# Kernel optimization log

Measured on AMD Instinct MI355X. Metric: run time of the kernel, lower is better.

Reference implementation:

```python
import jax, jax.numpy as jnp
import numpy as np

B, N, H = 8192, 8, 1024  # batch, DOF, hidden width; state dim = 2*N


def setup_inputs() -> dict:
    key = jax.random.key(0)
    ks = jax.random.split(key, 4)
    s1 = 1.0 / np.sqrt(2 * N)
    s2 = 1.0 / np.sqrt(H)
    return {
        "x": jax.random.normal(ks[0], (B, 2 * N), dtype=jnp.float32),
        "W1": jax.random.normal(ks[1], (2 * N, H), dtype=jnp.float32) * s1,
        "b1": jnp.zeros((H,), dtype=jnp.float32),
        "W2": jax.random.normal(ks[2], (H, H), dtype=jnp.float32) * s2,
        "b2": jnp.zeros((H,), dtype=jnp.float32),
        "W3": jax.random.normal(ks[3], (H, 1), dtype=jnp.float32) * s2,
        "b3": jnp.zeros((1,), dtype=jnp.float32),
    }


def reference(x, W1, b1, W2, b2, W3, b3):
    def lagrangian(q, qd):
        z = jnp.concatenate([q, qd])           # (2N,)
        h = jax.nn.softplus(z @ W1 + b1)
        h = jax.nn.softplus(h @ W2 + b2)
        return (h @ W3 + b3).sum()             # scalar L(q, qd)

    dL_dq_fn = jax.grad(lagrangian, argnums=0)
    dL_dqd_fn = jax.grad(lagrangian, argnums=1)
    # forward-over-reverse Hessian blocks (cheap: only N tangents)
    H_qdqd_fn = jax.jacfwd(dL_dqd_fn, argnums=1)   # d2L/dqd dqd, (N,N)
    H_qddq_fn = jax.jacfwd(dL_dqd_fn, argnums=0)   # d2L/dqd dq,  (N,N)

    def step(xi):
        q, qd = xi[:N], xi[N:]
        dL_dq = dL_dq_fn(q, qd)                      # (N,)
        M = H_qdqd_fn(q, qd)                         # mass-matrix block
        C = H_qddq_fn(q, qd)
        qdd = jnp.linalg.inv(M) @ (dL_dq - C @ qd)   # (N,)
        return jnp.concatenate([qd, qdd])            # (2N,)

    return jax.vmap(step)(x)
```

## Files before the change

### kernel.cpp

```cpp
#include <hip/hip_runtime.h>
#include <math.h>

#define B_ 8192
#define H_ 1024
#define LDP0 136
#define LDT 148

#define A_SEC 145
#define B2_SEC 257
#define A_GRN (12*A_SEC)
#define B2_GRN (12*B2_SEC)
#define AB2_SH ((A_GRN + B2_GRN)*8)

typedef short bfrag __attribute__((ext_vector_type(8)));
typedef float f4v  __attribute__((ext_vector_type(4)));

union U8 { unsigned short u[8]; uint4 v; };

__device__ __forceinline__ float sigf(float x){ return 1.0f/(1.0f+__expf(-x)); }

__device__ __forceinline__ unsigned int pkhi(unsigned int u1, unsigned int u0){
  return __builtin_amdgcn_perm(u1, u0, 0x07060302u);
}

__device__ __forceinline__ void gload_lds16(const void* g, void* l){
  __builtin_amdgcn_global_load_lds(
      (const __attribute__((address_space(1))) void*)g,
      (__attribute__((address_space(3))) void*)l, 16, 0, 0);
}

__global__ void k1_s1(const float* __restrict__ x, const float* __restrict__ W1,
                      const float* __restrict__ b1, float* __restrict__ s1o){
  __shared__ float xs[16];
  int b = blockIdx.x, t = threadIdx.x;
  if(t < 16) xs[t] = x[b*16 + t];
  __syncthreads();
  for(int h = t; h < H_; h += 256){
    float acc = b1[h];
    #pragma unroll
    for(int j=0;j<16;j++) acc = __fmaf_rn(xs[j], W1[j*H_ + h], acc);
    s1o[(size_t)b*H_ + h] = sigf(acc);
  }
}

__global__ __launch_bounds__(256,3) void k2_s2(const float* __restrict__ s1,
                      const float* __restrict__ W2, const float* __restrict__ b2,
                      float* __restrict__ s2o){
  __shared__ __align__(16) float As[32*LDP0];
  __shared__ __align__(16) float Bs[32*LDP0];
  int t = threadIdx.x, tx = t & 15, ty = t >> 4;
  int m0 = blockIdx.x * 128, n0 = blockIdx.y * 128;
  int jj = t & 31, rb4 = (t >> 5) * 4;
  float acc[8][8];
  #pragma unroll
  for(int i=0;i<8;i++){
    #pragma unroll
    for(int k=0;k<8;k++) acc[i][k]=0.f; }

  for(int jt=0; jt<32; jt++){
    int j0 = jt*32;
    __syncthreads();
    #pragma unroll
    for(int g=0; g<4; g++){
      #pragma unroll
      for(int i=0;i<4;i++){
        int r = rb4 + i + 32*g;
        As[jj*LDP0 + r] = -__logf(1.0f - s1[(size_t)(m0+r)*H_ + j0 + jj]);
      }
    }
    { int jB = t >> 3, kb = (t & 7) * 16;
      const float* src = &W2[(size_t)(j0 + jB)*H_ + n0 + kb];
      #pragma unroll
      for(int c=0;c<4;c++) *(float4*)&Bs[jB*LDP0 + kb + 4*c] = *(const float4*)(src + 4*c);
    }
    __syncthreads();
    #pragma unroll 8
    for(int j=0;j<32;j++){
      float4 a0 = *(const float4*)&As[j*LDP0 + 8*ty];
      float4 a1f= *(const float4*)&As[j*LDP0 + 8*ty+4];
      float4 b0 = *(const float4*)&Bs[j*LDP0 + 4*tx];
      float4 b1f= *(const float4*)&Bs[j*LDP0 + 64 + 4*tx];
      float aa[8] = {a0.x,a0.y,a0.z,a0.w,a1f.x,a1f.y,a1f.z,a1f.w};
      float bb[8] = {b0.x,b0.y,b0.z,b0.w,b1f.x,b1f.y,b1f.z,b1f.w};
      #pragma unroll
      for(int i=0;i<8;i++){
        #pragma unroll
        for(int k=0;k<8;k++) acc[i][k] = __fmaf_rn(aa[i], bb[k], acc[i][k]); }
    }
  }
  float4 bb0 = *(const float4*)&b2[n0 + 4*tx];
  float4 bb1 = *(const float4*)&b2[n0 + 64 + 4*tx];
  #pragma unroll
  for(int i=0;i<8;i++){
    size_t r = (size_t)(m0 + 8*ty + i)*H_;
    float4 o0 = make_float4(sigf(acc[i][0]+bb0.x), sigf(acc[i][1]+bb0.y),
                            sigf(acc[i][2]+bb0.z), sigf(acc[i][3]+bb0.w));
    float4 o1 = make_float4(sigf(acc[i][4]+bb1.x), sigf(acc[i][5]+bb1.y),
                            sigf(acc[i][6]+bb1.z), sigf(acc[i][7]+bb1.w));
    *(float4*)&s2o[r + n0 + 4*tx] = o0;
    *(float4*)&s2o[r + n0 + 64 + 4*tx] = o1;
  }
}

__global__ __launch_bounds__(256,3) void k3_u(const float* __restrict__ s2,
                      const float* __restrict__ W2, const float* __restrict__ W3,
                      float* __restrict__ u){
  __shared__ __align__(16) float As[32*LDP0];
  __shared__ __align__(16) float Bs[32*LDP0];
  int t = threadIdx.x, tx = t & 15, ty = t >> 4;
  int m0 = blockIdx.x * 128, n0 = blockIdx.y * 128;
  int jj = t & 31, rb4 = (t >> 5) * 4;
  float acc[8][8];
  #pragma unroll
  for(int i=0;i<8;i++){
    #pragma unroll
    for(int k=0;k<8;k++) acc[i][k]=0.f; }

  for(int kt=0; kt<32; kt++){
    int k0 = kt*32;
    __syncthreads();
    float w3v = W3[k0 + jj];
    #pragma unroll
    for(int g=0; g<4; g++){
      #pragma unroll
      for(int i=0;i<4;i++){
        int r = rb4 + i + 32*g;
        As[jj*LDP0 + r] = w3v * s2[(size_t)(m0+r)*H_ + k0 + jj];
      }
    }
    { int jcol = t >> 1, kb = (t & 1) * 16;
      const float* src = &W2[(size_t)(n0 + jcol)*H_ + k0 + kb];
      #pragma unroll
      for(int c=0;c<16;c++) Bs[(kb+c)*LDP0 + jcol] = src[c];
    }
    __syncthreads();
    #pragma unroll 8
    for(int j=0;j<32;j++){
      float4 a0 = *(const float4*)&As[j*LDP0 + 8*ty];
      float4 a1f= *(const float4*)&As[j*LDP0 + 8*ty+4];
      float4 b0 = *(const float4*)&Bs[j*LDP0 + 4*tx];
      float4 b1f= *(const float4*)&Bs[j*LDP0 + 64 + 4*tx];
      float aa[8] = {a0.x,a0.y,a0.z,a0.w,a1f.x,a1f.y,a1f.z,a1f.w};
      float bb[8] = {b0.x,b0.y,b0.z,b0.w,b1f.x,b1f.y,b1f.z,b1f.w};
      #pragma unroll
      for(int i=0;i<8;i++){
        #pragma unroll
        for(int k=0;k<8;k++) acc[i][k] = __fmaf_rn(aa[i], bb[k], acc[i][k]); }
    }
  }
  #pragma unroll
  for(int i=0;i<8;i++){
    size_t r = (size_t)(m0 + 8*ty + i)*H_;
    *(float4*)&u[r + n0 + 4*tx]      = make_float4(acc[i][0],acc[i][1],acc[i][2],acc[i][3]);
    *(float4*)&u[r + n0 + 64 + 4*tx] = make_float4(acc[i][4],acc[i][5],acc[i][6],acc[i][7]);
  }
}

__global__ void kF(const float* __restrict__ W1, float* __restrict__ F64){
  int e = blockIdx.x*256 + threadIdx.x;
  int j = e >> 6, p = e & 63;
  F64[e] = W1[(8+(p>>3))*H_ + j] * W1[(8+(p&7))*H_ + j];
}

__global__ __launch_bounds__(256) void k5a(const float* __restrict__ s1,
                      const float* __restrict__ u, const float* __restrict__ F64,
                      float* __restrict__ Hz1M){
  __shared__ __align__(16) float As[32*72];
  __shared__ __align__(16) float Bs[32*72];
  int t = threadIdx.x, tx = t & 15, ty = t >> 4;
  int m0 = blockIdx.x * 64;
  int jj = t & 31, rb8 = (t >> 5) * 8;
  float acc[4][4];
  #pragma unroll
  for(int i=0;i<4;i++){
    #pragma unroll
    for(int k=0;k<4;k++) acc[i][k]=0.f; }

  for(int jt=0; jt<32; jt++){
    int j0 = jt*32;
    __syncthreads();
    #pragma unroll
    for(int g=0; g<8; g++){
      int r = rb8 + g;
      float s = s1[(size_t)(m0+r)*H_ + j0 + jj];
      As[jj*72 + r] = s*(1.0f-s)*u[(size_t)(m0+r)*H_ + j0 + jj];
    }
    { int jB = t >> 3, cb = (t & 7) * 8;
      const float* src = &F64[(j0 + jB)*64 + cb];
      *(float4*)&Bs[jB*72 + cb]   = *(const float4*)(src);
      *(float4*)&Bs[jB*72 + cb+4] = *(const float4*)(src+4);
    }
    __syncthreads();
    #pragma unroll 8
    for(int j=0;j<32;j++){
      float4 a4 = *(const float4*)&As[j*72 + 4*ty];
      float4 b4 = *(const float4*)&Bs[j*72 + 4*tx];
      float aa[4] = {a4.x,a4.y,a4.z,a4.w};
      float bb[4] = {b4.x,b4.y,b4.z,b4.w};
      #pragma unroll
      for(int i=0;i<4;i++){
        #pragma unroll
        for(int k=0;k<4;k++) acc[i][k] = __fmaf_rn(aa[i], bb[k], acc[i][k]); }
    }
  }
  #pragma unroll
  for(int i=0;i<4;i++)
    *(float4*)&Hz1M[(size_t)(m0+4*ty+i)*64 + 4*tx] =
      make_float4(acc[i][0],acc[i][1],acc[i][2],acc[i][3]);
}

__global__ void k5b(const float* __restrict__ s1, const float* __restrict__ u,
                    const float* __restrict__ W1, const float* __restrict__ x,
                    float* __restrict__ dq16){
  int wid = threadIdx.x >> 6, lane = threadIdx.x & 63;
  int b = blockIdx.x*4 + wid;
  float qd[8];
  #pragma unroll
  for(int i=0;i<8;i++) qd[i] = x[b*16 + 8 + i];
  float accd[8] = {0,0,0,0,0,0,0,0};
  float accc[8] = {0,0,0,0,0,0,0,0};
  for(int jb=0;jb<16;jb++){
    int j = jb*64 + lane;
    float s1v = s1[(size_t)b*H_+j], uv = u[(size_t)b*H_+j];
    float g1 = s1v*uv;
    float d1 = (1.0f - s1v)*g1;
    float w1q = 0.f;
    #pragma unroll
    for(int i=0;i<8;i++){ float w = W1[i*H_+j];
      accd[i] = __fmaf_rn(g1, w, accd[i]);
      w1q = __fmaf_rn(qd[i], w, w1q); }
    float dw = d1*w1q;
    #pragma unroll
    for(int m=0;m<8;m++) accc[m] = __fmaf_rn(dw, W1[(8+m)*H_+j], accc[m]);
  }
  #pragma unroll
  for(int i=0;i<8;i++){
    #pragma unroll
    for(int off=1; off<64; off<<=1){
      accd[i] += __shfl_xor(accd[i], off, 64);
      accc[i] += __shfl_xor(accc[i], off, 64);
    }
  }
  if(lane==0){
    #pragma unroll
    for(int i=0;i<8;i++){ dq16[b*16+i] = accd[i]; dq16[b*16+8+i] = accc[i]; }
  }
}

__global__ void kW2T(const float* __restrict__ W2, unsigned short* __restrict__ Wh,
                     unsigned short* __restrict__ Wm, unsigned short* __restrict__ Wl){
  __shared__ float tile[32][132];
  int j0 = blockIdx.x * 32, k0 = blockIdx.y * 128;
  int t = threadIdx.x;
  int lr = t >> 3, lc0 = (t & 7) * 16;
  const float* src = &W2[(size_t)(j0+lr)*H_ + k0 + lc0];
  #pragma unroll
  for(int c=0;c<16;c+=4) *(float4*)&tile[lr][lc0+c] = *(const float4*)(src + c);
  __syncthreads();
  int k = t >> 1;
  #pragma unroll
  for(int o2=0;o2<2;o2++){
    int oc = (t&1)*2 + o2;
    U8 uh, um2, ul2;
    #pragma unroll
    for(int e=0;e<8;e++){
      float a = tile[oc*8+e][k];
      unsigned int ua = __float_as_uint(a);
      unsigned int h = ua & 0xFFFF0000u;
      float r1 = __fsub_rn(a, __uint_as_float(h));
      unsigned int m = __float_as_uint(r1) & 0xFFFF0000u;
      float l = __fsub_rn(r1, __uint_as_float(m));
      uh.u[e]  = (unsigned short)(h >> 16);
      um2.u[e] = (unsigned short)(m >> 16);
      ul2.u[e] = (unsigned short)(__float_as_uint(l) >> 16);
    }
    size_t o = (size_t)(k0+k)*H_ + j0 + oc*8;
    *(uint4*)&Wh[o] = uh.v; *(uint4*)&Wm[o] = um2.v; *(uint4*)&Wl[o] = ul2.v;
  }
}

__global__ __launch_bounds__(256,2) void k4_mfma(
    const float* __restrict__ s1, const float* __restrict__ s2,
    const float* __restrict__ x,  const float* __restrict__ W1,
    const unsigned short* __restrict__ W2Th, const unsigned short* __restrict__ W2Tm,
    const unsigned short* __restrict__ W2Tl,
    const float* __restrict__ W3, float* __restrict__ Mpart){
  __shared__ union {
    unsigned short AB[AB2_SH];
    float Td[64*LDT];
  } sm;
  __shared__ float qds[16][8];

  int t = threadIdx.x;
  int wv = t >> 6, lane = t & 63;
  int kb2 = blockIdx.x & 3, sgp = blockIdx.x >> 2;
  int b0 = sgp*16, k0 = kb2*256;

  if(t < 128){ int s = t>>3, i = t&7; qds[s][i] = x[(b0+s)*16 + 8+i]; }

  f4v acc[9][4];
  #pragma unroll
  for(int mt=0;mt<9;mt++){
    #pragma unroll
    for(int n2=0;n2<4;n2++){ acc[mt][n2][0]=0.f; acc[mt][n2][1]=0.f; acc[mt][n2][2]=0.f; acc[mt][n2][3]=0.f; }
  }

  int aoct = t & 3, arow = t >> 2;
  int fr_m = lane & 15, fr_q = lane >> 4;
  int pfm   = fr_m ^ ((fr_m & 8) >> 1);
  int aRd   = fr_q*A_SEC + pfm;
  int bRd   = A_GRN + fr_q*B2_SEC + wv*64 + pfm;
  int bsrow = ((wv*12) % 4)*0;

  for(int jt=0; jt<32; jt++){
    int j0 = jt*32;
    __syncthreads();
    {
      #pragma unroll
      for(int i=0;i<12;i++){
        int fid = wv*12 + i;
        int p = fid >> 4, rem = fid & 15;
        int oc = rem >> 2, run = rem & 3;
        int g  = run*64 + lane;
        int row = g ^ ((g & 8) >> 1);
        const unsigned short* gp = (p==0) ? W2Th : ((p==1) ? W2Tm : W2Tl);
        const unsigned short* ga = &gp[(size_t)(k0+row)*H_ + j0 + oc*8];
        unsigned short* la = (unsigned short*)&sm.AB[(size_t)(A_GRN + (p*4+oc)*B2_SEC + run*64)*8];
        gload_lds16(ga, la);
      }
    }
    #pragma unroll
    for(int pass=0; pass<3; pass++){
      int r = pass*64 + arow;
      if(r < 144){
        float4 w0, w1v, sa, sb;
        if(r < 128){
          int s = r>>3, m = r&7;
          const float* wp = &W1[(size_t)(8+m)*H_ + j0 + aoct*8];
          w0 = *(const float4*)wp; w1v = *(const float4*)(wp+4);
          const float* sp = &s1[(size_t)(b0+s)*H_ + j0 + aoct*8];
          sa = *(const float4*)sp; sb = *(const float4*)(sp+4);
        } else {
          int s = r - 128;
          float g0=0,g1=0,g2=0,g3=0,g4=0,g5=0,g6=0,g7=0;
          #pragma unroll
          for(int i=0;i<8;i++){
            float q = qds[s][i];
            const float* wp = &W1[(size_t)i*H_ + j0 + aoct*8];
            float4 a0 = *(const float4*)wp, a1 = *(const float4*)(wp+4);
            g0 = __fmaf_rn(q, a0.x, g0); g1 = __fmaf_rn(q, a0.y, g1);
            g2 = __fmaf_rn(q, a0.z, g2); g3 = __fmaf_rn(q, a0.w, g3);
            g4 = __fmaf_rn(q, a1.x, g4); g5 = __fmaf_rn(q, a1.y, g5);
            g6 = __fmaf_rn(q, a1.z, g6); g7 = __fmaf_rn(q, a1.w, g7);
          }
          w0 = make_float4(g0,g1,g2,g3); w1v = make_float4(g4,g5,g6,g7);
          const float* sp = &s1[(size_t)(b0+s)*H_ + j0 + aoct*8];
          sa = *(const float4*)sp; sb = *(const float4*)(sp+4);
        }
        float av[8];
        av[0]=__fmul_rn(w0.x,sa.x); av[1]=__fmul_rn(w0.y,sa.y);
        av[2]=__fmul_rn(w0.z,sa.z); av[3]=__fmul_rn(w0.w,sa.w);
        av[4]=__fmul_rn(w1v.x,sb.x); av[5]=__fmul_rn(w1v.y,sb.y);
        av[6]=__fmul_rn(w1v.z,sb.z); av[7]=__fmul_rn(w1v.w,sb.w);
        unsigned int uh[8], um[8], ul[8];
        #pragma unroll
        for(int e=0;e<8;e++){
          unsigned int ua = __float_as_uint(av[e]);
          unsigned int h = ua & 0xFFFF0000u;
          float r1 = __fsub_rn(av[e], __uint_as_float(h));
          unsigned int m = __float_as_uint(r1) & 0xFFFF0000u;
          float l = __fsub_rn(r1, __uint_as_float(m));
          uh[e]=h; um[e]=m; ul[e]=__float_as_uint(l);
        }
        int g0i = aoct*A_SEC + (r ^ ((r & 8) >> 1));
        uint4 vh = make_uint4(pkhi(uh[1],uh[0]), pkhi(uh[3],uh[2]), pkhi(uh[5],uh[4]), pkhi(uh[7],uh[6]));
        uint4 vm = make_uint4(pkhi(um[1],um[0]), pkhi(um[3],um[2]), pkhi(um[5],um[4]), pkhi(um[7],um[6]));
        uint4 vl = make_uint4(pkhi(ul[1],ul[0]), pkhi(ul[3],ul[2]), pkhi(ul[5],ul[4]), pkhi(ul[7],ul[6]));
        *(uint4*)&sm.AB[(g0i            )*8] = vh;
        *(uint4*)&sm.AB[(g0i + 4*A_SEC  )*8] = vm;
        *(uint4*)&sm.AB[(g0i + 8*A_SEC  )*8] = vl;
      }
    }
    __syncthreads();
    bfrag bf[4][3];
    #pragma unroll
    for(int n2=0;n2<4;n2++){
      #pragma unroll
      for(int p=0;p<3;p++) bf[n2][p] = *(bfrag*)&sm.AB[(bRd + p*4*B2_SEC + n2*16)*8];
    }
    #pragma unroll
    for(int mt=0; mt<9; mt++){
      bfrag a0 = *(bfrag*)&sm.AB[(aRd             + mt*16)*8];
      bfrag a1v= *(bfrag*)&sm.AB[(aRd + 4*A_SEC   + mt*16)*8];
      bfrag a2v= *(bfrag*)&sm.AB[(aRd + 8*A_SEC   + mt*16)*8];
      #pragma unroll
      for(int n2=0;n2<4;n2++){
        f4v c = acc[mt][n2];
        c = __builtin_amdgcn_mfma_f32_16x16x32_bf16(a2v, bf[n2][1], c, 0,0,0);
        c = __builtin_amdgcn_mfma_f32_16x16x32_bf16(a1v, bf[n2][2], c, 0,0,0);
        c = __builtin_amdgcn_mfma_f32_16x16x32_bf16(a2v, bf[n2][0], c, 0,0,0);
        c = __builtin_amdgcn_mfma_f32_16x16x32_bf16(a0,  bf[n2][2], c, 0,0,0);
        c = __builtin_amdgcn_mfma_f32_16x16x32_bf16(a1v, bf[n2][1], c, 0,0,0);
        c = __builtin_amdgcn_mfma_f32_16x16x32_bf16(a1v, bf[n2][0], c, 0,0,0);
        c = __builtin_amdgcn_mfma_f32_16x16x32_bf16(a0,  bf[n2][1], c, 0,0,0);
        c = __builtin_amdgcn_mfma_f32_16x16x32_bf16(a0,  bf[n2][0], c, 0,0,0);
        acc[mt][n2] = c;
      }
    }
  }

  float Mp[44];
  #pragma unroll
  for(int i=0;i<44;i++) Mp[i]=0.f;
  int es = t>>4, ec = t&15;
  const float* s2p = &s2[(size_t)(b0+es)*H_ + k0];

  #pragma unroll
  for(int ph=0; ph<4; ph++){
    __syncthreads();
    if(wv == ph){
      #pragma unroll
      for(int mt=0; mt<9; mt++){
        #pragma unroll
        for(int n2=0;n2<4;n2++){
          int col = n2*16 + fr_m;
          int rowb = mt*16 + fr_q*4;
          #pragma unroll
          for(int rg=0;rg<4;rg++)
            sm.Td[col*LDT + rowb + rg] = acc[mt][n2][rg];
        }
      }
    }
    __syncthreads();
    float4 s2v = *(const float4*)&s2p[ph*64 + ec*4];
    float4 w3v = *(const float4*)&W3[k0 + ph*64 + ec*4];
    float dv[4] = { w3v.x*s2v.x*(1.f-s2v.x), w3v.y*s2v.y*(1.f-s2v.y),
                    w3v.z*s2v.z*(1.f-s2v.z), w3v.w*s2v.w*(1.f-s2v.w) };
    #pragma unroll
    for(int e=0;e<4;e++){
      int col = ec*4+e;
      const float* tp = &sm.Td[col*LDT + es*8];
      float4 t0 = *(const float4*)tp, t1 = *(const float4*)(tp+4);
      float T8[8] = {t0.x,t0.y,t0.z,t0.w,t1.x,t1.y,t1.z,t1.w};
      float vv = sm.Td[col*LDT + 128 + es];
      float d = dv[e];
      int ix=0;
      #pragma unroll
      for(int m=0;m<8;m++){
        float w = __fmul_rn(T8[m], d);
        Mp[36+m] = __fmaf_rn(w, vv, Mp[36+m]);
        #pragma unroll
        for(int n=m;n<8;n++){ Mp[ix] = __fmaf_rn(w, T8[n], Mp[ix]); ix++; }
      }
    }
    if(ph & 1){
      #pragma unroll
      for(int i=0;i<44;i++){
        #pragma unroll
        for(int off=1; off<16; off<<=1) Mp[i] += __shfl_xor(Mp[i], off, 64);
      }
      if(ec==0){
        int kb = kb2*2 + (ph>>1);
        float* o = &Mpart[((size_t)(b0+es)*8 + kb)*44];
        #pragma unroll
        for(int i=0;i<44;i++) o[i] = Mp[i];
      }
      #pragma unroll
      for(int i=0;i<44;i++) Mp[i]=0.f;
    }
  }
}

__global__ __launch_bounds__(64) void k6(const float* __restrict__ x,
                    const float* __restrict__ Hz1M, const float* __restrict__ Mpart,
                    const float* __restrict__ dq16, float* __restrict__ out){
  __shared__ double A[64][73];
  int t = threadIdx.x;
  int b = blockIdx.x*64 + t;
  double* Ar = A[t];
  float qd[8];
  #pragma unroll
  for(int j=0;j<8;j++) qd[j] = x[b*16 + 8 + j];
  double Ms[44];
  #pragma unroll
  for(int i=0;i<44;i++) Ms[i]=0.0;
  for(int kb=0;kb<8;kb++){
    const float* mp = &Mpart[((size_t)b*8+kb)*44];
    #pragma unroll
    for(int i=0;i<44;i++) Ms[i] += (double)mp[i];
  }
  #pragma unroll
  for(int i=0;i<8;i++){
    #pragma unroll
    for(int j=0;j<8;j++) Ar[i*9+j] = (double)Hz1M[(size_t)b*64 + i*8 + j];
    Ar[i*9+8] = (double)dq16[b*16+i] - (double)dq16[b*16+8+i] - Ms[36+i];
  }
  { int ix=0;
    for(int m=0;m<8;m++)
      for(int n=m;n<8;n++){
        Ar[m*9+n] += Ms[ix];
        if(n>m) Ar[n*9+m] += Ms[ix];
        ix++;
      }
  }
  for(int c=0;c<8;c++){
    int piv = c; double best = fabs(Ar[c*9+c]);
    for(int rr=c+1; rr<8; rr++){ double v = fabs(Ar[rr*9+c]); if(v>best){best=v;piv=rr;} }
    if(piv!=c){
      for(int cc=c; cc<9; cc++){ double tmp=Ar[c*9+cc]; Ar[c*9+cc]=Ar[piv*9+cc]; Ar[piv*9+cc]=tmp; }
    }
    double inv = 1.0/Ar[c*9+c];
    for(int rr=c+1; rr<8; rr++){
      double f = Ar[rr*9+c]*inv;
      for(int cc=c+1; cc<9; cc++) Ar[rr*9+cc] -= f*Ar[c*9+cc];
    }
  }
  double sol[8];
  #pragma unroll
  for(int i=7;i>=0;i--){
    double s = Ar[i*9+8];
    #pragma unroll
    for(int j=i+1;j<8;j++) s -= Ar[i*9+j]*sol[j];
    sol[i] = s/Ar[i*9+i];
  }
  #pragma unroll
  for(int j=0;j<8;j++) out[b*16+j] = qd[j];
  #pragma unroll
  for(int i=0;i<8;i++) out[b*16+8+i] = (float)sol[i];
}

extern "C" void kernel_launch(void* const* d_in, const int* in_sizes, int n_in,
                              void* d_out, int out_size, void* d_ws, size_t ws_size,
                              hipStream_t stream){
  const float* x  = (const float*)d_in[0];
  const float* W1 = (const float*)d_in[1];
  const float* b1 = (const float*)d_in[2];
  const float* W2 = (const float*)d_in[3];
  const float* b2 = (const float*)d_in[4];
  const float* W3 = (const float*)d_in[5];
  float* out = (float*)d_out;

  float* ws   = (float*)d_ws;
  size_t BH   = (size_t)B_*H_;
  float* s1   = ws;
  float* s2   = s1  + BH;
  float* u    = s2  + BH;
  float* F64  = u   + BH;
  float* Hz1M = F64 + (size_t)H_*64;
  float* dq16 = Hz1M+ (size_t)B_*64;

  float* Mpart = u;
  unsigned short* W2Th = (unsigned short*)(u + 3145728);
  unsigned short* W2Tm = W2Th + (size_t)H_*H_;
  unsigned short* W2Tl = W2Tm + (size_t)H_*H_;

  k1_s1 <<<dim3(B_),      dim3(256), 0, stream>>>(x, W1, b1, s1);
  k2_s2 <<<dim3(64,8),    dim3(256), 0, stream>>>(s1, W2, b2, s2);
  k3_u  <<<dim3(64,8),    dim3(256), 0, stream>>>(s2, W2, W3, u);
  kF    <<<dim3(256),     dim3(256), 0, stream>>>(W1, F64);
  k5a   <<<dim3(128),     dim3(256), 0, stream>>>(s1, u, F64, Hz1M);
  k5b   <<<dim3(2048),    dim3(256), 0, stream>>>(s1, u, W1, x, dq16);
  kW2T  <<<dim3(32,8),    dim3(256), 0, stream>>>(W2, W2Th, W2Tm, W2Tl);
  k4_mfma<<<dim3(2048),   dim3(256), 0, stream>>>(s1, s2, x, W1, W2Th, W2Tm, W2Tl, W3, Mpart);
  k6    <<<dim3(128),     dim3(64),  0, stream>>>(x, Hz1M, Mpart, dq16, out);
}
```

Measured before the change: 1.957 ms.

## Interleave A-tile split construction with MFMA blocks and drop leading barrier

The main k-loop no longer waits at a barrier before issuing the W2 global-to-LDS loads. Only A-tile rows 0..63 are built up front. Rows 64..143 (the s1*W1 products and the qd-projected rows) are now computed and split into bf16 parts between the first MFMA row-blocks, with the barrier moved to after MT_BLOCK(3). The aim is to hide VALU and global-load latency behind matrix-core work and remove one barrier per iteration, at the cost of a more delicate LDS hazard ordering and more live registers.

```diff
diff --git a/kernel.cpp b/kernel.cpp
--- a/kernel.cpp
+++ b/kernel.cpp
@@ -278,6 +278,50 @@
     *(uint4*)&Wh[o] = uh.v; *(uint4*)&Wm[o] = um2.v; *(uint4*)&Wl[o] = ul2.v;
   }
 }
+
+#define SPLIT_STORE(R, W0, W1V, SA, SB) do{ \
+  float av[8]; \
+  av[0]=__fmul_rn((W0).x,(SA).x); av[1]=__fmul_rn((W0).y,(SA).y); \
+  av[2]=__fmul_rn((W0).z,(SA).z); av[3]=__fmul_rn((W0).w,(SA).w); \
+  av[4]=__fmul_rn((W1V).x,(SB).x); av[5]=__fmul_rn((W1V).y,(SB).y); \
+  av[6]=__fmul_rn((W1V).z,(SB).z); av[7]=__fmul_rn((W1V).w,(SB).w); \
+  unsigned int uh[8], um[8], ul[8]; \
+  _Pragma("unroll") \
+  for(int e=0;e<8;e++){ \
+    unsigned int ua = __float_as_uint(av[e]); \
+    unsigned int h = ua & 0xFFFF0000u; \
+    float r1_ = __fsub_rn(av[e], __uint_as_float(h)); \
+    unsigned int m_ = __float_as_uint(r1_) & 0xFFFF0000u; \
+    float l_ = __fsub_rn(r1_, __uint_as_float(m_)); \
+    uh[e]=h; um[e]=m_; ul[e]=__float_as_uint(l_); \
+  } \
+  int g0i = aoct*A_SEC + ((R) ^ (((R) & 8) >> 1)); \
+  uint4 vh = make_uint4(pkhi(uh[1],uh[0]), pkhi(uh[3],uh[2]), pkhi(uh[5],uh[4]), pkhi(uh[7],uh[6])); \
+  uint4 vm = make_uint4(pkhi(um[1],um[0]), pkhi(um[3],um[2]), pkhi(um[5],um[4]), pkhi(um[7],um[6])); \
+  uint4 vl = make_uint4(pkhi(ul[1],ul[0]), pkhi(ul[3],ul[2]), pkhi(ul[5],ul[4]), pkhi(ul[7],ul[6])); \
+  *(uint4*)&sm.AB[(g0i          )*8] = vh; \
+  *(uint4*)&sm.AB[(g0i + 4*A_SEC)*8] = vm; \
+  *(uint4*)&sm.AB[(g0i + 8*A_SEC)*8] = vl; \
+}while(0)
+
+#define MT_BLOCK(MT) do{ \
+  bfrag a0 = *(bfrag*)&sm.AB[(aRd            + (MT)*16)*8]; \
+  bfrag a1v= *(bfrag*)&sm.AB[(aRd + 4*A_SEC  + (MT)*16)*8]; \
+  bfrag a2v= *(bfrag*)&sm.AB[(aRd + 8*A_SEC  + (MT)*16)*8]; \
+  _Pragma("unroll") \
+  for(int n2=0;n2<4;n2++){ \
+    f4v c = acc[(MT)][n2]; \
+    c = __builtin_amdgcn_mfma_f32_16x16x32_bf16(a2v, bf[n2][1], c, 0,0,0); \
+    c = __builtin_amdgcn_mfma_f32_16x16x32_bf16(a1v, bf[n2][2], c, 0,0,0); \
+    c = __builtin_amdgcn_mfma_f32_16x16x32_bf16(a2v, bf[n2][0], c, 0,0,0); \
+    c = __builtin_amdgcn_mfma_f32_16x16x32_bf16(a0,  bf[n2][2], c, 0,0,0); \
+    c = __builtin_amdgcn_mfma_f32_16x16x32_bf16(a1v, bf[n2][1], c, 0,0,0); \
+    c = __builtin_amdgcn_mfma_f32_16x16x32_bf16(a1v, bf[n2][0], c, 0,0,0); \
+    c = __builtin_amdgcn_mfma_f32_16x16x32_bf16(a0,  bf[n2][1], c, 0,0,0); \
+    c = __builtin_amdgcn_mfma_f32_16x16x32_bf16(a0,  bf[n2][0], c, 0,0,0); \
+    acc[(MT)][n2] = c; \
+  } \
+}while(0)
 
 __global__ __launch_bounds__(256,2) void k4_mfma(
     const float* __restrict__ s1, const float* __restrict__ s2,
@@ -310,76 +354,28 @@
   int pfm   = fr_m ^ ((fr_m & 8) >> 1);
   int aRd   = fr_q*A_SEC + pfm;
   int bRd   = A_GRN + fr_q*B2_SEC + wv*64 + pfm;
-  int bsrow = ((wv*12) % 4)*0;
 
   for(int jt=0; jt<32; jt++){
     int j0 = jt*32;
-    __syncthreads();
+    #pragma unroll
+    for(int i=0;i<12;i++){
+      int fid = wv*12 + i;
+      int p = fid >> 4, rem = fid & 15;
+      int oc = rem >> 2, run = rem & 3;
+      int g  = run*64 + lane;
+      int row = g ^ ((g & 8) >> 1);
+      const unsigned short* gp = (p==0) ? W2Th : ((p==1) ? W2Tm : W2Tl);
+      gload_lds16(&gp[(size_t)(k0+row)*H_ + j0 + oc*8],
+                  (unsigned short*)&sm.AB[(size_t)(A_GRN + (p*4+oc)*B2_SEC + run*64)*8]);
+    }
     {
-      #pragma unroll
-      for(int i=0;i<12;i++){
-        int fid = wv*12 + i;
-        int p = fid >> 4, rem = fid & 15;
-        int oc = rem >> 2, run = rem & 3;
-        int g  = run*64 + lane;
-        int row = g ^ ((g & 8) >> 1);
-        const unsigned short* gp = (p==0) ? W2Th : ((p==1) ? W2Tm : W2Tl);
-        const unsigned short* ga = &gp[(size_t)(k0+row)*H_ + j0 + oc*8];
-        unsigned short* la = (unsigned short*)&sm.AB[(size_t)(A_GRN + (p*4+oc)*B2_SEC + run*64)*8];
-        gload_lds16(ga, la);
-      }
-    }
-    #pragma unroll
-    for(int pass=0; pass<3; pass++){
-      int r = pass*64 + arow;
-      if(r < 144){
-        float4 w0, w1v, sa, sb;
-        if(r < 128){
-          int s = r>>3, m = r&7;
-          const float* wp = &W1[(size_t)(8+m)*H_ + j0 + aoct*8];
-          w0 = *(const float4*)wp; w1v = *(const float4*)(wp+4);
-          const float* sp = &s1[(size_t)(b0+s)*H_ + j0 + aoct*8];
-          sa = *(const float4*)sp; sb = *(const float4*)(sp+4);
-        } else {
-          int s = r - 128;
-          float g0=0,g1=0,g2=0,g3=0,g4=0,g5=0,g6=0,g7=0;
-          #pragma unroll
-          for(int i=0;i<8;i++){
-            float q = qds[s][i];
-            const float* wp = &W1[(size_t)i*H_ + j0 + aoct*8];
-            float4 a0 = *(const float4*)wp, a1 = *(const float4*)(wp+4);
-            g0 = __fmaf_rn(q, a0.x, g0); g1 = __fmaf_rn(q, a0.y, g1);
-            g2 = __fmaf_rn(q, a0.z, g2); g3 = __fmaf_rn(q, a0.w, g3);
-            g4 = __fmaf_rn(q, a1.x, g4); g5 = __fmaf_rn(q, a1.y, g5);
-            g6 = __fmaf_rn(q, a1.z, g6); g7 = __fmaf_rn(q, a1.w, g7);
-          }
-          w0 = make_float4(g0,g1,g2,g3); w1v = make_float4(g4,g5,g6,g7);
-          const float* sp = &s1[(size_t)(b0+s)*H_ + j0 + aoct*8];
-          sa = *(const float4*)sp; sb = *(const float4*)(sp+4);
-        }
-        float av[8];
-        av[0]=__fmul_rn(w0.x,sa.x); av[1]=__fmul_rn(w0.y,sa.y);
-        av[2]=__fmul_rn(w0.z,sa.z); av[3]=__fmul_rn(w0.w,sa.w);
-        av[4]=__fmul_rn(w1v.x,sb.x); av[5]=__fmul_rn(w1v.y,sb.y);
-        av[6]=__fmul_rn(w1v.z,sb.z); av[7]=__fmul_rn(w1v.w,sb.w);
-        unsigned int uh[8], um[8], ul[8];
-        #pragma unroll
-        for(int e=0;e<8;e++){
-          unsigned int ua = __float_as_uint(av[e]);
-          unsigned int h = ua & 0xFFFF0000u;
-          float r1 = __fsub_rn(av[e], __uint_as_float(h));
-          unsigned int m = __float_as_uint(r1) & 0xFFFF0000u;
-          float l = __fsub_rn(r1, __uint_as_float(m));
-          uh[e]=h; um[e]=m; ul[e]=__float_as_uint(l);
-        }
-        int g0i = aoct*A_SEC + (r ^ ((r & 8) >> 1));
-        uint4 vh = make_uint4(pkhi(uh[1],uh[0]), pkhi(uh[3],uh[2]), pkhi(uh[5],uh[4]), pkhi(uh[7],uh[6]));
-        uint4 vm = make_uint4(pkhi(um[1],um[0]), pkhi(um[3],um[2]), pkhi(um[5],um[4]), pkhi(um[7],um[6]));
-        uint4 vl = make_uint4(pkhi(ul[1],ul[0]), pkhi(ul[3],ul[2]), pkhi(ul[5],ul[4]), pkhi(ul[7],ul[6]));
-        *(uint4*)&sm.AB[(g0i            )*8] = vh;
-        *(uint4*)&sm.AB[(g0i + 4*A_SEC  )*8] = vm;
-        *(uint4*)&sm.AB[(g0i + 8*A_SEC  )*8] = vl;
-      }
+      int r = arow;
+      int s = r>>3, m = r&7;
+      const float* wp = &W1[(size_t)(8+m)*H_ + j0 + aoct*8];
+      float4 w0 = *(const float4*)wp, w1v = *(const float4*)(wp+4);
+      const float* sp = &s1[(size_t)(b0+s)*H_ + j0 + aoct*8];
+      float4 sa = *(const float4*)sp, sb = *(const float4*)(sp+4);
+      SPLIT_STORE(r, w0, w1v, sa, sb);
     }
     __syncthreads();
     bfrag bf[4][3];
@@ -388,25 +384,45 @@
       #pragma unroll
       for(int p=0;p<3;p++) bf[n2][p] = *(bfrag*)&sm.AB[(bRd + p*4*B2_SEC + n2*16)*8];
     }
-    #pragma unroll
-    for(int mt=0; mt<9; mt++){
-      bfrag a0 = *(bfrag*)&sm.AB[(aRd             + mt*16)*8];
-      bfrag a1v= *(bfrag*)&sm.AB[(aRd + 4*A_SEC   + mt*16)*8];
-      bfrag a2v= *(bfrag*)&sm.AB[(aRd + 8*A_SEC   + mt*16)*8];
-      #pragma unroll
-      for(int n2=0;n2<4;n2++){
-        f4v c = acc[mt][n2];
-        c = __builtin_amdgcn_mfma_f32_16x16x32_bf16(a2v, bf[n2][1], c, 0,0,0);
-        c = __builtin_amdgcn_mfma_f32_16x16x32_bf16(a1v, bf[n2][2], c, 0,0,0);
-        c = __builtin_amdgcn_mfma_f32_16x16x32_bf16(a2v, bf[n2][0], c, 0,0,0);
-        c = __builtin_amdgcn_mfma_f32_16x16x32_bf16(a0,  bf[n2][2], c, 0,0,0);
-        c = __builtin_amdgcn_mfma_f32_16x16x32_bf16(a1v, bf[n2][1], c, 0,0,0);
-        c = __builtin_amdgcn_mfma_f32_16x16x32_bf16(a1v, bf[n2][0], c, 0,0,0);
-        c = __builtin_amdgcn_mfma_f32_16x16x32_bf16(a0,  bf[n2][1], c, 0,0,0);
-        c = __builtin_amdgcn_mfma_f32_16x16x32_bf16(a0,  bf[n2][0], c, 0,0,0);
-        acc[mt][n2] = c;
-      }
-    }
+    int r1 = 64 + arow;
+    float4 p1w0, p1w1, p1sa, p1sb;
+    {
+      int s = r1>>3, m = r1&7;
+      const float* wp = &W1[(size_t)(8+m)*H_ + j0 + aoct*8];
+      p1w0 = *(const float4*)wp; p1w1 = *(const float4*)(wp+4);
+      const float* sp = &s1[(size_t)(b0+s)*H_ + j0 + aoct*8];
+      p1sa = *(const float4*)sp; p1sb = *(const float4*)(sp+4);
+    }
+    MT_BLOCK(0);
+    SPLIT_STORE(r1, p1w0, p1w1, p1sa, p1sb);
+    MT_BLOCK(1);
+    if(t < 64){
+      int r2 = 128 + arow;
+      int s = r2 - 128;
+      float g0=0,g1=0,g2=0,g3=0,g4=0,g5=0,g6=0,g7=0;
+      #pragma unroll
+      for(int i=0;i<8;i++){
+        float q = qds[s][i];
+        const float* wp = &W1[(size_t)i*H_ + j0 + aoct*8];
+        float4 a0 = *(const float4*)wp, a1 = *(const float4*)(wp+4);
+        g0 = __fmaf_rn(q, a0.x, g0); g1 = __fmaf_rn(q, a0.y, g1);
+        g2 = __fmaf_rn(q, a0.z, g2); g3 = __fmaf_rn(q, a0.w, g3);
+        g4 = __fmaf_rn(q, a1.x, g4); g5 = __fmaf_rn(q, a1.y, g5);
+        g6 = __fmaf_rn(q, a1.z, g6); g7 = __fmaf_rn(q, a1.w, g7);
+      }
+      float4 w0 = make_float4(g0,g1,g2,g3), w1v = make_float4(g4,g5,g6,g7);
+      const float* sp = &s1[(size_t)(b0+s)*H_ + j0 + aoct*8];
+      float4 sa = *(const float4*)sp, sb = *(const float4*)(sp+4);
+      SPLIT_STORE(r2, w0, w1v, sa, sb);
+    }
+    MT_BLOCK(2);
+    MT_BLOCK(3);
+    __syncthreads();
+    MT_BLOCK(4);
+    MT_BLOCK(5);
+    MT_BLOCK(6);
+    MT_BLOCK(7);
+    MT_BLOCK(8);
   }
 
   float Mp[44];
```

Result: slower. 2.198 ms (+12.4%).
